# Kernel optimization log

Hardware: AMD Instinct MI355X
Metric: run time of the kernel (lower is better)

The kernel has to match this reference:

```python
import jax, jax.numpy as jnp
import numpy as np

N = 50000      # nodes
E = 1600000    # message edges (avg degree 32)
EQ = 500000    # link-prediction query edges
IN, HID, OUT, FCH = 128, 128, 64, 256
ALPHA = 0.5


def setup_inputs() -> dict:
    key = jax.random.key(0)
    ks = jax.random.split(key, 8)
    def p(k, shape):
        fan_in = shape[0]
        return jax.random.normal(k, shape, jnp.float32) * (1.0 / np.sqrt(fan_in))
    return {
        "x": jax.random.normal(ks[0], (N, IN), jnp.float32),
        "edge_index": jax.random.randint(ks[1], (2, E), 0, N),
        "edge_label_index": jax.random.randint(ks[2], (2, EQ), 0, N),
        "W1": p(ks[3], (IN, HID)),  "b1": jnp.zeros((HID,), jnp.float32),
        "W2": p(ks[4], (HID, OUT)), "b2": jnp.zeros((OUT,), jnp.float32),
        "Wf1": p(ks[5], (IN, FCH)), "bf1": jnp.zeros((FCH,), jnp.float32),
        "Wf2": p(ks[6], (FCH, OUT)), "bf2": jnp.zeros((OUT,), jnp.float32),
    }


def reference(x, edge_index, edge_label_index, W1, b1, W2, b2, Wf1, bf1, Wf2, bf2):
    n = x.shape[0]
    # GCN self-loops + symmetric normalization (PyG GCNConv defaults)
    loop = jnp.arange(n)
    src = jnp.concatenate([edge_index[0], loop])
    dst = jnp.concatenate([edge_index[1], loop])
    deg = jax.ops.segment_sum(jnp.ones_like(dst, jnp.float32), dst, num_segments=n)
    dinv = jnp.where(deg > 0, jax.lax.rsqrt(deg), 0.0)
    norm = dinv[src] * dinv[dst]  # [E+N]

    def gcn(h, W, b):
        h = h @ W                                  # transform first (PyG order)
        msg = norm[:, None] * h[src]               # gather + scale per edge
        return jax.ops.segment_sum(msg, dst, num_segments=n) + b

    x_gcn = jax.nn.relu(gcn(x, W1, b1))
    x_gcn = gcn(x_gcn, W2, b2)
    x_fc = jax.nn.relu(x @ Wf1 + bf1) @ Wf2 + bf2
    z = x_gcn * (1.0 - ALPHA) + x_fc * ALPHA       # [N, OUT]
    # edge dot-product decode
    return jnp.sum(z[edge_label_index[0]] * z[edge_label_index[1]], axis=1)
```

## Files before the change

kernel.cpp:

```cpp
#include <hip/hip_runtime.h>

#define FIN   128
#define FHID  128
#define FOUT  64
#define FFC   256
#define CHUNK 4096
#define BKBITS 7
#define BKN   128
#define ECAP  4608

typedef __attribute__((ext_vector_type(8))) short          bf16x8;
typedef __attribute__((ext_vector_type(4))) float          f32x4;
typedef __attribute__((ext_vector_type(2))) float          f32x2;
typedef __attribute__((ext_vector_type(8))) unsigned short u16x8;

static __device__ __forceinline__ unsigned short f2bf(float f) {
    unsigned int u = __float_as_uint(f);
    u = (u + 0x7fffu + ((u >> 16) & 1u)) >> 16;
    return (unsigned short)u;
}
static __device__ __forceinline__ float bf2f(unsigned short s) {
    return __uint_as_float(((unsigned int)s) << 16);
}
static __device__ __forceinline__ void accum_fp8(float* acc, uint4 g) {
    f32x2 p;
    p = __builtin_amdgcn_cvt_pk_f32_fp8(g.x, false); acc[0]  += p.x; acc[1]  += p.y;
    p = __builtin_amdgcn_cvt_pk_f32_fp8(g.x, true);  acc[2]  += p.x; acc[3]  += p.y;
    p = __builtin_amdgcn_cvt_pk_f32_fp8(g.y, false); acc[4]  += p.x; acc[5]  += p.y;
    p = __builtin_amdgcn_cvt_pk_f32_fp8(g.y, true);  acc[6]  += p.x; acc[7]  += p.y;
    p = __builtin_amdgcn_cvt_pk_f32_fp8(g.z, false); acc[8]  += p.x; acc[9]  += p.y;
    p = __builtin_amdgcn_cvt_pk_f32_fp8(g.z, true);  acc[10] += p.x; acc[11] += p.y;
    p = __builtin_amdgcn_cvt_pk_f32_fp8(g.w, false); acc[12] += p.x; acc[13] += p.y;
    p = __builtin_amdgcn_cvt_pk_f32_fp8(g.w, true);  acc[14] += p.x; acc[15] += p.y;
}

__global__ __launch_bounds__(256) void binA_cvt_kernel(
    const int* __restrict__ src, const int* __restrict__ dst,
    int* __restrict__ bcur, unsigned int* __restrict__ ebuf, int E, int NBA,
    const float* __restrict__ W1, const float* __restrict__ W2,
    const float* __restrict__ Wf1, const float* __restrict__ Wf2,
    unsigned short* __restrict__ w1t, unsigned short* __restrict__ w2t,
    unsigned short* __restrict__ wf1t, unsigned short* __restrict__ wf2t)
{
    int t = threadIdx.x;
    if (blockIdx.x >= NBA) {
        long i = (long)(blockIdx.x - NBA) * 256 + t;
        if (i < 16384) {
            int k = (int)i >> 7, n = (int)i & 127;
            w1t[n * 128 + k] = f2bf(W1[i]);
        } else if (i < 24576) {
            int j = (int)i - 16384; int k = j >> 6, n = j & 63;
            w2t[n * 128 + k] = f2bf(W2[j]);
        } else if (i < 57344) {
            int j = (int)i - 24576; int k = j >> 8, n = j & 255;
            wf1t[n * 128 + k] = f2bf(Wf1[j]);
        } else if (i < 73728) {
            int j = (int)i - 57344; int k = j >> 6, n = j & 63;
            wf2t[n * 256 + k] = f2bf(Wf2[j]);
        }
        return;
    }
    __shared__ int hist[512];
    __shared__ int rstart[512];
    __shared__ int lcur[512];
    hist[t] = 0; hist[t + 256] = 0; lcur[t] = 0; lcur[t + 256] = 0;
    __syncthreads();
    int e0 = blockIdx.x * CHUNK;
    int e1 = min(e0 + CHUNK, E);
    for (int e = e0 + t; e < e1; e += 256)
        atomicAdd(&hist[dst[e] >> BKBITS], 1);
    __syncthreads();
    if (hist[t])       rstart[t]       = atomicAdd(&bcur[t],       hist[t]);
    if (hist[t + 256]) rstart[t + 256] = atomicAdd(&bcur[t + 256], hist[t + 256]);
    __syncthreads();
    for (int e = e0 + t; e < e1; e += 256) {
        int s = src[e], d = dst[e];
        int b = d >> BKBITS;
        int pos = rstart[b] + atomicAdd(&lcur[b], 1);
        if (pos < ECAP)
            ebuf[(size_t)b * ECAP + pos] =
                ((unsigned)s << BKBITS) | ((unsigned)d & (BKN - 1));
    }
}

__global__ __launch_bounds__(256) void binB_fc_kernel(
    const unsigned int* __restrict__ ebuf, const int* __restrict__ bcnt,
    int2* __restrict__ rp2, int* __restrict__ col, float* __restrict__ dinv,
    unsigned char* __restrict__ xs, int N, int NBK,
    const float* __restrict__ X,
    const unsigned short* __restrict__ B1T,
    const unsigned short* __restrict__ B2T,
    const float* __restrict__ bias1, const float* __restrict__ bias2,
    unsigned short* __restrict__ C, int M)
{
    __shared__ __align__(16) unsigned char smem[49152];
    const int tid = threadIdx.x;

    if (blockIdx.x < NBK) {
        int* cnt           = (int*)smem;
        int* tmp           = (int*)(smem + 512);
        int* ccur          = (int*)(smem + 1536);
        int* scur          = (int*)(smem + 2048);
        float* sdinv       = (float*)(smem + 3072);
        unsigned int* skey = (unsigned int*)(smem + 3584);
        int* colLds        = (int*)(smem + 22016);
        int b = blockIdx.x;
        int t = tid;
        size_t base = (size_t)b * ECAP;
        int ne = min(bcnt[b], ECAP);
        if (t < 128) cnt[t] = 0;
        scur[t] = 0;
        __syncthreads();
        for (int e = t; e < ne; e += 256) {
            unsigned int k = ebuf[base + e];
            atomicAdd(&cnt[k & (BKN - 1)], 1);
            atomicAdd(&scur[k >> 15], 1);
        }
        __syncthreads();
        int c = (t < 128) ? cnt[t] : 0;
        tmp[t] = c;
        __syncthreads();
        int acc = c;
        for (int off = 1; off < 128; off <<= 1) {
            int a = (t >= off) ? tmp[t - off] : 0;
            __syncthreads();
            acc += a; tmp[t] = acc;
            __syncthreads();
        }
        if (t < 128) {
            float di = rsqrtf((float)c + 1.0f);
            sdinv[t] = di;
            int node = b * BKN + t;
            int st = (int)base + acc - c;
            if (node < N) { dinv[node] = di; rp2[node] = make_int2(st, st + c); }
            ccur[t] = acc - c;
        }
        __syncthreads();
        int sv = scur[t];
        tmp[t] = sv;
        __syncthreads();
        int sacc = sv;
        for (int off = 1; off < 256; off <<= 1) {
            int a = (t >= off) ? tmp[t - off] : 0;
            __syncthreads();
            sacc += a; tmp[t] = sacc;
            __syncthreads();
        }
        scur[t] = sacc - sv;
        __syncthreads();
        for (int e = t; e < ne; e += 256) {
            unsigned int k = ebuf[base + e];
            int pos = atomicAdd(&scur[k >> 15], 1);
            skey[pos] = k;
        }
        __syncthreads();
        for (int w = 0; w < ne; w += 256) {
            int e = w + t;
            if (e < ne) {
                unsigned int k = skey[e];
                int pos = atomicAdd(&ccur[k & (BKN - 1)], 1);
                colLds[pos] = (int)(k >> BKBITS);
            }
            __syncthreads();
        }
        for (int e = t; e < ne; e += 256)
            col[base + e] = colLds[e];
        int nl0 = t >> 3;
        int f0 = (t & 7) << 4;
        #pragma unroll
        for (int it = 0; it < 4; it++) {
            int nl = it * 32 + nl0;
            int gn = b * BKN + nl;
            if (gn >= N) continue;
            float d2 = sdinv[nl];
            const float* xr = X + (size_t)gn * FIN + f0;
            float4 va = *(const float4*)(xr);
            float4 vb = *(const float4*)(xr + 4);
            float4 vc = *(const float4*)(xr + 8);
            float4 vd = *(const float4*)(xr + 12);
            float f[16] = { va.x * d2, va.y * d2, va.z * d2, va.w * d2,
                            vb.x * d2, vb.y * d2, vb.z * d2, vb.w * d2,
                            vc.x * d2, vc.y * d2, vc.z * d2, vc.w * d2,
                            vd.x * d2, vd.y * d2, vd.z * d2, vd.w * d2 };
            uint4 w;
            w.x = 0; w.y = 0; w.z = 0; w.w = 0;
            w.x = __builtin_amdgcn_cvt_pk_fp8_f32(f[0],  f[1],  w.x, false);
            w.x = __builtin_amdgcn_cvt_pk_fp8_f32(f[2],  f[3],  w.x, true);
            w.y = __builtin_amdgcn_cvt_pk_fp8_f32(f[4],  f[5],  w.y, false);
            w.y = __builtin_amdgcn_cvt_pk_fp8_f32(f[6],  f[7],  w.y, true);
            w.z = __builtin_amdgcn_cvt_pk_fp8_f32(f[8],  f[9],  w.z, false);
            w.z = __builtin_amdgcn_cvt_pk_fp8_f32(f[10], f[11], w.z, true);
            w.w = __builtin_amdgcn_cvt_pk_fp8_f32(f[12], f[13], w.w, false);
            w.w = __builtin_amdgcn_cvt_pk_fp8_f32(f[14], f[15], w.w, true);
            *(uint4*)(xs + (size_t)gn * 128 + f0) = w;
        }
        return;
    }

    unsigned short* lds = (unsigned short*)smem;
    const int lane = tid & 63;
    const int wave = tid >> 6;
    const int m = lane & 15;
    const int q = lane >> 4;
    const int rowbase = (blockIdx.x - NBK) * 64 + wave * 16;
    const int row = rowbase + m;

    float4 av[8] = {};
    {
        const float* arow = X + (size_t)row * FIN + q * 8;
        if (row < M) {
            #pragma unroll
            for (int kk = 0; kk < 4; kk++) {
                av[2 * kk]     = *(const float4*)(arow + kk * 32);
                av[2 * kk + 1] = *(const float4*)(arow + kk * 32 + 4);
            }
        }
    }

    #pragma unroll 2
    for (int i = tid; i < 2048; i += 256) {
        int n = i >> 4, sl = i & 15;
        ((u16x8*)lds)[(n << 4) | (sl ^ (n & 7))] = ((const u16x8*)B1T)[i];
    }
    __syncthreads();

    f32x4 acc[16] = {};
    for (int k0 = 0; k0 < 128; k0 += 32) {
        int kk = k0 >> 5;
        float4 a0 = av[2 * kk], a1 = av[2 * kk + 1];
        bf16x8 a;
        a[0] = (short)f2bf(a0.x); a[1] = (short)f2bf(a0.y);
        a[2] = (short)f2bf(a0.z); a[3] = (short)f2bf(a0.w);
        a[4] = (short)f2bf(a1.x); a[5] = (short)f2bf(a1.y);
        a[6] = (short)f2bf(a1.z); a[7] = (short)f2bf(a1.w);
        int sl = q + (k0 >> 3);
        #pragma unroll
        for (int c = 0; c < 8; c++) {
            int cc = c * 16 + m;
            bf16x8 b = ((const bf16x8*)lds)[(cc << 4) | (sl ^ (cc & 7))];
            acc[c] = __builtin_amdgcn_mfma_f32_16x16x32_bf16(a, b, acc[c], 0, 0, 0);
        }
    }
    __syncthreads();
    #pragma unroll 2
    for (int i = tid; i < 2048; i += 256) {
        int n = i >> 4, sl = i & 15;
        ((u16x8*)lds)[(n << 4) | (sl ^ (n & 7))] = ((const u16x8*)B1T)[2048 + i];
    }
    __syncthreads();
    for (int k0 = 0; k0 < 128; k0 += 32) {
        int kk = k0 >> 5;
        float4 a0 = av[2 * kk], a1 = av[2 * kk + 1];
        bf16x8 a;
        a[0] = (short)f2bf(a0.x); a[1] = (short)f2bf(a0.y);
        a[2] = (short)f2bf(a0.z); a[3] = (short)f2bf(a0.w);
        a[4] = (short)f2bf(a1.x); a[5] = (short)f2bf(a1.y);
        a[6] = (short)f2bf(a1.z); a[7] = (short)f2bf(a1.w);
        int sl = q + (k0 >> 3);
        #pragma unroll
        for (int c = 0; c < 8; c++) {
            int cc = c * 16 + m;
            bf16x8 b = ((const bf16x8*)lds)[(cc << 4) | (sl ^ (cc & 7))];
            acc[8 + c] = __builtin_amdgcn_mfma_f32_16x16x32_bf16(a, b, acc[8 + c], 0, 0, 0);
        }
    }
    __syncthreads();
    #pragma unroll
    for (int c = 0; c < 16; c++) {
        int cc = c * 16 + m;
        float bv = bias1[cc];
        #pragma unroll
        for (int r = 0; r < 4; r++) {
            int rr = wave * 16 + q * 4 + r;
            float v = fmaxf(acc[c][r] + bv, 0.f);
            lds[rr * 256 + ((((cc >> 3) ^ (rr & 7)) << 3) | (cc & 7))] = f2bf(v);
        }
    }
    for (int i = tid; i < 1024; i += 256) {
        int n = i >> 4, sl = i & 15;
        ((u16x8*)lds)[2048 + ((n << 4) | (sl ^ (n & 7)))] =
            ((const u16x8*)B2T)[n * 32 + sl];
    }
    __syncthreads();

    f32x4 acc2[4] = {};
    {
        int rr = wave * 16 + m;
        for (int k0 = 0; k0 < 128; k0 += 32) {
            int sl = q + (k0 >> 3);
            bf16x8 a = ((const bf16x8*)lds)[(rr << 5) | (sl ^ (rr & 7))];
            #pragma unroll
            for (int c = 0; c < 4; c++) {
                int cc = c * 16 + m;
                bf16x8 b = ((const bf16x8*)lds)[2048 + ((cc << 4) | (sl ^ (cc & 7)))];
                acc2[c] = __builtin_amdgcn_mfma_f32_16x16x32_bf16(a, b, acc2[c], 0, 0, 0);
            }
        }
    }
    __syncthreads();
    for (int i = tid; i < 1024; i += 256) {
        int n = i >> 4, sl = i & 15;
        ((u16x8*)lds)[2048 + ((n << 4) | (sl ^ (n & 7)))] =
            ((const u16x8*)B2T)[n * 32 + 16 + sl];
    }
    __syncthreads();
    {
        int rr = wave * 16 + m;
        for (int k0 = 128; k0 < 256; k0 += 32) {
            int sla = q + (k0 >> 3);
            int slb = q + ((k0 - 128) >> 3);
            bf16x8 a = ((const bf16x8*)lds)[(rr << 5) | (sla ^ (rr & 7))];
            #pragma unroll
            for (int c = 0; c < 4; c++) {
                int cc = c * 16 + m;
                bf16x8 b = ((const bf16x8*)lds)[2048 + ((cc << 4) | (slb ^ (cc & 7)))];
                acc2[c] = __builtin_amdgcn_mfma_f32_16x16x32_bf16(a, b, acc2[c], 0, 0, 0);
            }
        }
    }
    __syncthreads();

    constexpr int ROWB = 4 * 16 * 2 + 16;
    unsigned char* wbase = (unsigned char*)lds + wave * 16 * ROWB;
    #pragma unroll
    for (int c = 0; c < 4; c++) {
        int lc = c * 16 + m;
        float bv = bias2[lc];
        #pragma unroll
        for (int r = 0; r < 4; r++)
            ((unsigned short*)(wbase + (q * 4 + r) * ROWB))[lc] =
                f2bf(acc2[c][r] + bv);
    }
    #pragma unroll
    for (int p = 0; p < 2; p++) {
        int r2 = p * 8 + (lane >> 3);
        int bo = (lane & 7) * 16;
        int gr = rowbase + r2;
        if (gr < M) {
            uint4 v = *(const uint4*)(wbase + r2 * ROWB + bo);
            *(uint4*)((unsigned char*)C + (size_t)gr * FOUT * 2 + bo) = v;
        }
    }
}

__global__ __launch_bounds__(256) void pull1_kernel(
    const unsigned char* __restrict__ xs, const int2* __restrict__ rp2,
    const int* __restrict__ col, const float* __restrict__ dinv,
    unsigned short* __restrict__ aggx, int N)
{
    int tid = threadIdx.x;
    int node = blockIdx.x * 32 + (tid >> 3);
    if (node >= N) return;
    int f0 = (tid & 7) << 4;
    const unsigned char* base = xs + f0;
    float di = dinv[node];
    int2 se = rp2[node];
    float acc[16] = {};
    accum_fp8(acc, *(const uint4*)(base + (size_t)node * 128));
    int e = se.x, end = se.y;
    for (; e + 4 <= end; e += 4) {
        int s0 = col[e], s1 = col[e + 1], s2 = col[e + 2], s3 = col[e + 3];
        uint4 g0 = *(const uint4*)(base + (size_t)s0 * 128);
        uint4 g1 = *(const uint4*)(base + (size_t)s1 * 128);
        uint4 g2 = *(const uint4*)(base + (size_t)s2 * 128);
        uint4 g3 = *(const uint4*)(base + (size_t)s3 * 128);
        accum_fp8(acc, g0); accum_fp8(acc, g1);
        accum_fp8(acc, g2); accum_fp8(acc, g3);
    }
    for (; e < end; e++)
        accum_fp8(acc, *(const uint4*)(base + (size_t)col[e] * 128));
    u16x8 o0, o1;
    #pragma unroll
    for (int j = 0; j < 8; j++) {
        o0[j] = f2bf(di * acc[j]);
        o1[j] = f2bf(di * acc[8 + j]);
    }
    *(u16x8*)(aggx + (size_t)node * FIN + f0)     = o0;
    *(u16x8*)(aggx + (size_t)node * FIN + f0 + 8) = o1;
}

__global__ __launch_bounds__(256) void gcn_kernel(
    const unsigned short* __restrict__ A,
    const unsigned short* __restrict__ B1T,
    const unsigned short* __restrict__ B2T,
    const float* __restrict__ bias1,
    const float* __restrict__ rowscale,
    unsigned short* __restrict__ C, int M)
{
    __shared__ __align__(16) unsigned short lds[16384];
    const int tid  = threadIdx.x;
    const int lane = tid & 63;
    const int wave = tid >> 6;
    const int m = lane & 15;
    const int q = lane >> 4;
    const int rowbase = blockIdx.x * 64 + wave * 16;
    const int row = rowbase + m;

    bf16x8 areg[4] = {};
    {
        const unsigned short* arow = A + (size_t)row * FIN + q * 8;
        if (row < M) {
            #pragma unroll
            for (int kk = 0; kk < 4; kk++)
                areg[kk] = *(const bf16x8*)(arow + kk * 32);
        }
    }

    #pragma unroll 2
    for (int i = tid; i < 2048; i += 256) {
        int n = i >> 4, sl = i & 15;
        ((u16x8*)lds)[(n << 4) | (sl ^ (n & 7))] = ((const u16x8*)B1T)[i];
    }
    __syncthreads();

    f32x4 acc[8] = {};
    for (int k0 = 0; k0 < 128; k0 += 32) {
        bf16x8 a = areg[k0 >> 5];
        int sl = q + (k0 >> 3);
        #pragma unroll
        for (int c = 0; c < 8; c++) {
            int cc = c * 16 + m;
            bf16x8 b = ((const bf16x8*)lds)[(cc << 4) | (sl ^ (cc & 7))];
            acc[c] = __builtin_amdgcn_mfma_f32_16x16x32_bf16(a, b, acc[c], 0, 0, 0);
        }
    }
    __syncthreads();

    #pragma unroll
    for (int c = 0; c < 8; c++) {
        int cc = c * 16 + m;
        float bv = bias1[cc];
        #pragma unroll
        for (int r = 0; r < 4; r++) {
            int rr = wave * 16 + q * 4 + r;
            float v = fmaxf(acc[c][r] + bv, 0.f);
            lds[rr * 128 + ((((cc >> 3) ^ (rr & 7)) << 3) | (cc & 7))] = f2bf(v);
        }
    }
    for (int i = tid; i < 1024; i += 256) {
        int n = i >> 4, sl = i & 15;
        ((u16x8*)lds)[1024 + ((n << 4) | (sl ^ (n & 7)))] = ((const u16x8*)B2T)[i];
    }
    __syncthreads();

    f32x4 acc2[4] = {};
    {
        int rr = wave * 16 + m;
        for (int k0 = 0; k0 < 128; k0 += 32) {
            int sl = q + (k0 >> 3);
            bf16x8 a = ((const bf16x8*)lds)[(rr << 4) | (sl ^ (rr & 7))];
            #pragma unroll
            for (int c = 0; c < 4; c++) {
                int cc = c * 16 + m;
                bf16x8 b = ((const bf16x8*)lds)[1024 + ((cc << 4) | (sl ^ (cc & 7)))];
                acc2[c] = __builtin_amdgcn_mfma_f32_16x16x32_bf16(a, b, acc2[c], 0, 0, 0);
            }
        }
    }
    float rs[4];
    #pragma unroll
    for (int r = 0; r < 4; r++) {
        int gr = rowbase + q * 4 + r;
        rs[r] = (gr < M) ? rowscale[gr] : 1.0f;
    }
    __syncthreads();

    constexpr int ROWB = 4 * 16 * 2 + 16;
    unsigned char* wbase = (unsigned char*)lds + wave * 16 * ROWB;
    #pragma unroll
    for (int c = 0; c < 4; c++) {
        int lc = c * 16 + m;
        #pragma unroll
        for (int r = 0; r < 4; r++)
            ((unsigned short*)(wbase + (q * 4 + r) * ROWB))[lc] =
                f2bf(acc2[c][r] * rs[r]);
    }
    #pragma unroll
    for (int p = 0; p < 2; p++) {
        int r2 = p * 8 + (lane >> 3);
        int bo = (lane & 7) * 16;
        int gr = rowbase + r2;
        if (gr < M) {
            uint4 v = *(const uint4*)(wbase + r2 * ROWB + bo);
            *(uint4*)((unsigned char*)C + (size_t)gr * FOUT * 2 + bo) = v;
        }
    }
}

__global__ __launch_bounds__(256) void pull2_kernel(
    const unsigned short* __restrict__ t2s, const int2* __restrict__ rp2,
    const int* __restrict__ col, const float* __restrict__ dinv,
    const unsigned short* __restrict__ xfc, const float* __restrict__ b2,
    unsigned short* __restrict__ zbf, int N)
{
    int tid = threadIdx.x;
    int node = blockIdx.x * 32 + (tid >> 3);
    if (node >= N) return;
    int f0 = (tid & 7) << 3;
    const unsigned short* base = t2s + f0;
    float di = dinv[node];
    u16x8 xv = *(const u16x8*)(xfc + (size_t)node * FOUT + f0);
    float4 bb0 = *(const float4*)(b2 + f0);
    float4 bb1 = *(const float4*)(b2 + f0 + 4);
    u16x8 own = *(const u16x8*)(base + (size_t)node * FOUT);
    float acc[8];
    #pragma unroll
    for (int j = 0; j < 8; j++) acc[j] = bf2f(own[j]);
    int2 se = rp2[node];
    int e = se.x, end = se.y;
    for (; e + 4 <= end; e += 4) {
        int s0 = col[e], s1 = col[e + 1], s2 = col[e + 2], s3 = col[e + 3];
        u16x8 v0 = *(const u16x8*)(base + (size_t)s0 * FOUT);
        u16x8 v1 = *(const u16x8*)(base + (size_t)s1 * FOUT);
        u16x8 v2 = *(const u16x8*)(base + (size_t)s2 * FOUT);
        u16x8 v3 = *(const u16x8*)(base + (size_t)s3 * FOUT);
        #pragma unroll
        for (int j = 0; j < 8; j++)
            acc[j] += (bf2f(v0[j]) + bf2f(v1[j])) + (bf2f(v2[j]) + bf2f(v3[j]));
    }
    for (; e < end; e++) {
        u16x8 v = *(const u16x8*)(base + (size_t)col[e] * FOUT);
        #pragma unroll
        for (int j = 0; j < 8; j++) acc[j] += bf2f(v[j]);
    }
    float bv[8] = { bb0.x, bb0.y, bb0.z, bb0.w, bb1.x, bb1.y, bb1.z, bb1.w };
    u16x8 o;
    #pragma unroll
    for (int j = 0; j < 8; j++)
        o[j] = f2bf(0.5f * (di * acc[j] + bv[j]) + 0.5f * bf2f(xv[j]));
    *(u16x8*)(zbf + (size_t)node * FOUT + f0) = o;
}

__global__ void decode_kernel(
    const unsigned short* __restrict__ zbf, const int* __restrict__ eli,
    float* __restrict__ out, int Q)
{
    int tid = blockIdx.x * blockDim.x + threadIdx.x;
    int q = tid >> 3;
    if (q >= Q) return;
    int lane = tid & 7;
    int a = eli[q];
    int b = eli[Q + q];
    u16x8 va = *(const u16x8*)(zbf + (size_t)a * FOUT + lane * 8);
    u16x8 vb = *(const u16x8*)(zbf + (size_t)b * FOUT + lane * 8);
    float s = 0.f;
    #pragma unroll
    for (int j = 0; j < 8; j++) s += bf2f(va[j]) * bf2f(vb[j]);
    s += __shfl_down(s, 4, 8);
    s += __shfl_down(s, 2, 8);
    s += __shfl_down(s, 1, 8);
    if (lane == 0) out[q] = s;
}

extern "C" void kernel_launch(void* const* d_in, const int* in_sizes, int n_in,
                              void* d_out, int out_size, void* d_ws, size_t ws_size,
                              hipStream_t stream)
{
    const float* x   = (const float*)d_in[0];
    const int*   ei  = (const int*)  d_in[1];
    const int*   eli = (const int*)  d_in[2];
    const float* W1  = (const float*)d_in[3];
    const float* b1  = (const float*)d_in[4];
    const float* W2  = (const float*)d_in[5];
    const float* b2  = (const float*)d_in[6];
    const float* Wf1 = (const float*)d_in[7];
    const float* bf1 = (const float*)d_in[8];
    const float* Wf2 = (const float*)d_in[9];
    const float* bf2 = (const float*)d_in[10];
    float* out = (float*)d_out;

    const int N = in_sizes[0] / FIN;
    const int E = in_sizes[1] / 2;
    const int Q = in_sizes[2] / 2;
    const int* src = ei;
    const int* dst = ei + E;
    const int NBK = (N + BKN - 1) >> BKBITS;
    const int NBA = (E + CHUNK - 1) / CHUNK;
    const int NCV = 73728 / 256;
    const int NFC = (N + 63) / 64;

    char* p = (char*)d_ws;
    float* dinv = (float*)p;             p += (size_t)N * 4;
    int2*  rp2  = (int2*)p;              p += (size_t)N * 8;
    int*   bcur = (int*)p;               p += 2048;
    unsigned short* w1t  = (unsigned short*)p; p += FIN * FHID * 2;
    unsigned short* w2t  = (unsigned short*)p; p += FHID * FOUT * 2;
    unsigned short* wf1t = (unsigned short*)p; p += FIN * FFC * 2;
    unsigned short* wf2t = (unsigned short*)p; p += FFC * FOUT * 2;
    unsigned short* xfc = (unsigned short*)p;  p += (size_t)N * FOUT * 2;
    unsigned char* xs = (unsigned char*)p;     p += (size_t)N * 128;
    unsigned int* ebuf = (unsigned int*)p;  p += (size_t)NBK * ECAP * 4;
    int*   col  = (int*)p;               p += (size_t)NBK * ECAP * 4;
    unsigned short* aggx = (unsigned short*)p; p += (size_t)N * FIN * 2;
    unsigned short* t2s  = (unsigned short*)p; p += (size_t)N * FOUT * 2;
    unsigned short* zbf  = (unsigned short*)p; p += (size_t)N * FOUT * 2;

    const int TB = 256;

    hipMemsetAsync(bcur, 0, 2048, stream);

    binA_cvt_kernel<<<NBA + NCV, TB, 0, stream>>>(
        src, dst, bcur, ebuf, E, NBA,
        W1, W2, Wf1, Wf2, w1t, w2t, wf1t, wf2t);

    binB_fc_kernel<<<NBK + NFC, TB, 0, stream>>>(
        ebuf, bcur, rp2, col, dinv, xs, N, NBK,
        x, wf1t, wf2t, bf1, bf2, xfc, N);

    pull1_kernel<<<(N + 31) / 32, TB, 0, stream>>>(xs, rp2, col, dinv, aggx, N);

    gcn_kernel<<<(N + 63) / 64, TB, 0, stream>>>(
        aggx, w1t, w2t, b1, dinv, t2s, N);

    pull2_kernel<<<(N + 31) / 32, TB, 0, stream>>>(
        t2s, rp2, col, dinv, xfc, b2, zbf, N);

    {
        long total = (long)Q * 8;
        decode_kernel<<<(int)((total + TB - 1) / TB), TB, 0, stream>>>(
            zbf, eli, out, Q);
    }
}
```

Baseline: 242.4 us.

## Co-schedule edge binning with FC MLP and split weight conversion into own kernel

Weight conversion moves into its own small kernel. Edge pass A (histogram binning) now shares a launch with the FC MLP blocks, and bin pass B (CSR build plus fp8 x scaling) runs as a separate kernel afterwards. The binning pass also loads its 16 src/dst pairs per thread into registers once instead of reading global memory twice. The aim is to overlap the memory-bound binning with the compute-bound FC GEMM and cut redundant index loads, at the cost of one extra kernel launch.

```diff
diff --git a/kernel.cpp b/kernel.cpp
--- a/kernel.cpp
+++ b/kernel.cpp
@@ -34,59 +34,31 @@
     p = __builtin_amdgcn_cvt_pk_f32_fp8(g.w, true);  acc[14] += p.x; acc[15] += p.y;
 }
 
-__global__ __launch_bounds__(256) void binA_cvt_kernel(
-    const int* __restrict__ src, const int* __restrict__ dst,
-    int* __restrict__ bcur, unsigned int* __restrict__ ebuf, int E, int NBA,
+__global__ __launch_bounds__(256) void cvt_kernel(
     const float* __restrict__ W1, const float* __restrict__ W2,
     const float* __restrict__ Wf1, const float* __restrict__ Wf2,
     unsigned short* __restrict__ w1t, unsigned short* __restrict__ w2t,
     unsigned short* __restrict__ wf1t, unsigned short* __restrict__ wf2t)
 {
-    int t = threadIdx.x;
-    if (blockIdx.x >= NBA) {
-        long i = (long)(blockIdx.x - NBA) * 256 + t;
-        if (i < 16384) {
-            int k = (int)i >> 7, n = (int)i & 127;
-            w1t[n * 128 + k] = f2bf(W1[i]);
-        } else if (i < 24576) {
-            int j = (int)i - 16384; int k = j >> 6, n = j & 63;
-            w2t[n * 128 + k] = f2bf(W2[j]);
-        } else if (i < 57344) {
-            int j = (int)i - 24576; int k = j >> 8, n = j & 255;
-            wf1t[n * 128 + k] = f2bf(Wf1[j]);
-        } else if (i < 73728) {
-            int j = (int)i - 57344; int k = j >> 6, n = j & 63;
-            wf2t[n * 256 + k] = f2bf(Wf2[j]);
-        }
-        return;
-    }
-    __shared__ int hist[512];
-    __shared__ int rstart[512];
-    __shared__ int lcur[512];
-    hist[t] = 0; hist[t + 256] = 0; lcur[t] = 0; lcur[t + 256] = 0;
-    __syncthreads();
-    int e0 = blockIdx.x * CHUNK;
-    int e1 = min(e0 + CHUNK, E);
-    for (int e = e0 + t; e < e1; e += 256)
-        atomicAdd(&hist[dst[e] >> BKBITS], 1);
-    __syncthreads();
-    if (hist[t])       rstart[t]       = atomicAdd(&bcur[t],       hist[t]);
-    if (hist[t + 256]) rstart[t + 256] = atomicAdd(&bcur[t + 256], hist[t + 256]);
-    __syncthreads();
-    for (int e = e0 + t; e < e1; e += 256) {
-        int s = src[e], d = dst[e];
-        int b = d >> BKBITS;
-        int pos = rstart[b] + atomicAdd(&lcur[b], 1);
-        if (pos < ECAP)
-            ebuf[(size_t)b * ECAP + pos] =
-                ((unsigned)s << BKBITS) | ((unsigned)d & (BKN - 1));
-    }
-}
-
-__global__ __launch_bounds__(256) void binB_fc_kernel(
-    const unsigned int* __restrict__ ebuf, const int* __restrict__ bcnt,
-    int2* __restrict__ rp2, int* __restrict__ col, float* __restrict__ dinv,
-    unsigned char* __restrict__ xs, int N, int NBK,
+    long i = (long)blockIdx.x * 256 + threadIdx.x;
+    if (i < 16384) {
+        int k = (int)i >> 7, n = (int)i & 127;
+        w1t[n * 128 + k] = f2bf(W1[i]);
+    } else if (i < 24576) {
+        int j = (int)i - 16384; int k = j >> 6, n = j & 63;
+        w2t[n * 128 + k] = f2bf(W2[j]);
+    } else if (i < 57344) {
+        int j = (int)i - 24576; int k = j >> 8, n = j & 255;
+        wf1t[n * 128 + k] = f2bf(Wf1[j]);
+    } else if (i < 73728) {
+        int j = (int)i - 57344; int k = j >> 6, n = j & 63;
+        wf2t[n * 256 + k] = f2bf(Wf2[j]);
+    }
+}
+
+__global__ __launch_bounds__(256) void binA_fc_kernel(
+    const int* __restrict__ src, const int* __restrict__ dst,
+    int* __restrict__ bcur, unsigned int* __restrict__ ebuf, int E, int NBA,
     const float* __restrict__ X,
     const unsigned short* __restrict__ B1T,
     const unsigned short* __restrict__ B2T,
@@ -96,103 +68,41 @@
     __shared__ __align__(16) unsigned char smem[49152];
     const int tid = threadIdx.x;
 
-    if (blockIdx.x < NBK) {
-        int* cnt           = (int*)smem;
-        int* tmp           = (int*)(smem + 512);
-        int* ccur          = (int*)(smem + 1536);
-        int* scur          = (int*)(smem + 2048);
-        float* sdinv       = (float*)(smem + 3072);
-        unsigned int* skey = (unsigned int*)(smem + 3584);
-        int* colLds        = (int*)(smem + 22016);
-        int b = blockIdx.x;
+    if (blockIdx.x < NBA) {
+        int* hist   = (int*)smem;
+        int* rstart = (int*)(smem + 2048);
+        int* lcur   = (int*)(smem + 4096);
         int t = tid;
-        size_t base = (size_t)b * ECAP;
-        int ne = min(bcnt[b], ECAP);
-        if (t < 128) cnt[t] = 0;
-        scur[t] = 0;
-        __syncthreads();
-        for (int e = t; e < ne; e += 256) {
-            unsigned int k = ebuf[base + e];
-            atomicAdd(&cnt[k & (BKN - 1)], 1);
-            atomicAdd(&scur[k >> 15], 1);
-        }
-        __syncthreads();
-        int c = (t < 128) ? cnt[t] : 0;
-        tmp[t] = c;
-        __syncthreads();
-        int acc = c;
-        for (int off = 1; off < 128; off <<= 1) {
-            int a = (t >= off) ? tmp[t - off] : 0;
-            __syncthreads();
-            acc += a; tmp[t] = acc;
-            __syncthreads();
-        }
-        if (t < 128) {
-            float di = rsqrtf((float)c + 1.0f);
-            sdinv[t] = di;
-            int node = b * BKN + t;
-            int st = (int)base + acc - c;
-            if (node < N) { dinv[node] = di; rp2[node] = make_int2(st, st + c); }
-            ccur[t] = acc - c;
-        }
-        __syncthreads();
-        int sv = scur[t];
-        tmp[t] = sv;
-        __syncthreads();
-        int sacc = sv;
-        for (int off = 1; off < 256; off <<= 1) {
-            int a = (t >= off) ? tmp[t - off] : 0;
-            __syncthreads();
-            sacc += a; tmp[t] = sacc;
-            __syncthreads();
-        }
-        scur[t] = sacc - sv;
-        __syncthreads();
-        for (int e = t; e < ne; e += 256) {
-            unsigned int k = ebuf[base + e];
-            int pos = atomicAdd(&scur[k >> 15], 1);
-            skey[pos] = k;
-        }
-        __syncthreads();
-        for (int w = 0; w < ne; w += 256) {
-            int e = w + t;
-            if (e < ne) {
-                unsigned int k = skey[e];
-                int pos = atomicAdd(&ccur[k & (BKN - 1)], 1);
-                colLds[pos] = (int)(k >> BKBITS);
+        hist[t] = 0; hist[t + 256] = 0; lcur[t] = 0; lcur[t + 256] = 0;
+        __syncthreads();
+        int e0 = blockIdx.x * CHUNK;
+        int cnt_e = min(CHUNK, E - e0);
+        int sreg[16], dreg[16];
+        #pragma unroll
+        for (int i = 0; i < 16; i++) {
+            int o = t + i * 256;
+            bool ok = o < cnt_e;
+            sreg[i] = ok ? src[e0 + o] : 0;
+            dreg[i] = ok ? dst[e0 + o] : 0;
+            if (ok) ;
+        }
+        #pragma unroll
+        for (int i = 0; i < 16; i++)
+            if (t + i * 256 < cnt_e) atomicAdd(&hist[dreg[i] >> BKBITS], 1);
+        __syncthreads();
+        if (hist[t])       rstart[t]       = atomicAdd(&bcur[t],       hist[t]);
+        if (hist[t + 256]) rstart[t + 256] = atomicAdd(&bcur[t + 256], hist[t + 256]);
+        __syncthreads();
+        #pragma unroll
+        for (int i = 0; i < 16; i++) {
+            if (t + i * 256 < cnt_e) {
+                int s = sreg[i], d = dreg[i];
+                int b = d >> BKBITS;
+                int pos = rstart[b] + atomicAdd(&lcur[b], 1);
+                if (pos < ECAP)
+                    ebuf[(size_t)b * ECAP + pos] =
+                        ((unsigned)s << BKBITS) | ((unsigned)d & (BKN - 1));
             }
-            __syncthreads();
-        }
-        for (int e = t; e < ne; e += 256)
-            col[base + e] = colLds[e];
-        int nl0 = t >> 3;
-        int f0 = (t & 7) << 4;
-        #pragma unroll
-        for (int it = 0; it < 4; it++) {
-            int nl = it * 32 + nl0;
-            int gn = b * BKN + nl;
-            if (gn >= N) continue;
-            float d2 = sdinv[nl];
-            const float* xr = X + (size_t)gn * FIN + f0;
-            float4 va = *(const float4*)(xr);
-            float4 vb = *(const float4*)(xr + 4);
-            float4 vc = *(const float4*)(xr + 8);
-            float4 vd = *(const float4*)(xr + 12);
-            float f[16] = { va.x * d2, va.y * d2, va.z * d2, va.w * d2,
-                            vb.x * d2, vb.y * d2, vb.z * d2, vb.w * d2,
-                            vc.x * d2, vc.y * d2, vc.z * d2, vc.w * d2,
-                            vd.x * d2, vd.y * d2, vd.z * d2, vd.w * d2 };
-            uint4 w;
-            w.x = 0; w.y = 0; w.z = 0; w.w = 0;
-            w.x = __builtin_amdgcn_cvt_pk_fp8_f32(f[0],  f[1],  w.x, false);
-            w.x = __builtin_amdgcn_cvt_pk_fp8_f32(f[2],  f[3],  w.x, true);
-            w.y = __builtin_amdgcn_cvt_pk_fp8_f32(f[4],  f[5],  w.y, false);
-            w.y = __builtin_amdgcn_cvt_pk_fp8_f32(f[6],  f[7],  w.y, true);
-            w.z = __builtin_amdgcn_cvt_pk_fp8_f32(f[8],  f[9],  w.z, false);
-            w.z = __builtin_amdgcn_cvt_pk_fp8_f32(f[10], f[11], w.z, true);
-            w.w = __builtin_amdgcn_cvt_pk_fp8_f32(f[12], f[13], w.w, false);
-            w.w = __builtin_amdgcn_cvt_pk_fp8_f32(f[14], f[15], w.w, true);
-            *(uint4*)(xs + (size_t)gn * 128 + f0) = w;
         }
         return;
     }
@@ -202,7 +112,7 @@
     const int wave = tid >> 6;
     const int m = lane & 15;
     const int q = lane >> 4;
-    const int rowbase = (blockIdx.x - NBK) * 64 + wave * 16;
+    const int rowbase = (blockIdx.x - NBA) * 64 + wave * 16;
     const int row = rowbase + m;
 
     float4 av[8] = {};
@@ -340,6 +250,111 @@
             uint4 v = *(const uint4*)(wbase + r2 * ROWB + bo);
             *(uint4*)((unsigned char*)C + (size_t)gr * FOUT * 2 + bo) = v;
         }
+    }
+}
+
+__global__ __launch_bounds__(256) void binB_kernel(
+    const unsigned int* __restrict__ ebuf, const int* __restrict__ bcnt,
+    int2* __restrict__ rp2, int* __restrict__ col, float* __restrict__ dinv,
+    const float* __restrict__ x, unsigned char* __restrict__ xs, int N)
+{
+    __shared__ __align__(16) unsigned char smem[40448];
+    int* cnt           = (int*)smem;
+    int* tmp           = (int*)(smem + 512);
+    int* ccur          = (int*)(smem + 1536);
+    int* scur          = (int*)(smem + 2048);
+    float* sdinv       = (float*)(smem + 3072);
+    unsigned int* skey = (unsigned int*)(smem + 3584);
+    int* colLds        = (int*)(smem + 22016);
+    int b = blockIdx.x;
+    int t = threadIdx.x;
+    size_t base = (size_t)b * ECAP;
+    int ne = min(bcnt[b], ECAP);
+    if (t < 128) cnt[t] = 0;
+    scur[t] = 0;
+    __syncthreads();
+    for (int e = t; e < ne; e += 256) {
+        unsigned int k = ebuf[base + e];
+        atomicAdd(&cnt[k & (BKN - 1)], 1);
+        atomicAdd(&scur[k >> 15], 1);
+    }
+    __syncthreads();
+    int c = (t < 128) ? cnt[t] : 0;
+    tmp[t] = c;
+    __syncthreads();
+    int acc = c;
+    for (int off = 1; off < 128; off <<= 1) {
+        int a = (t >= off) ? tmp[t - off] : 0;
+        __syncthreads();
+        acc += a; tmp[t] = acc;
+        __syncthreads();
+    }
+    if (t < 128) {
+        float di = rsqrtf((float)c + 1.0f);
+        sdinv[t] = di;
+        int node = b * BKN + t;
+        int st = (int)base + acc - c;
+        if (node < N) { dinv[node] = di; rp2[node] = make_int2(st, st + c); }
+        ccur[t] = acc - c;
+    }
+    __syncthreads();
+    int sv = scur[t];
+    tmp[t] = sv;
+    __syncthreads();
+    int sacc = sv;
+    for (int off = 1; off < 256; off <<= 1) {
+        int a = (t >= off) ? tmp[t - off] : 0;
+        __syncthreads();
+        sacc += a; tmp[t] = sacc;
+        __syncthreads();
+    }
+    scur[t] = sacc - sv;
+    __syncthreads();
+    for (int e = t; e < ne; e += 256) {
+        unsigned int k = ebuf[base + e];
+        int pos = atomicAdd(&scur[k >> 15], 1);
+        skey[pos] = k;
+    }
+    __syncthreads();
+    for (int w = 0; w < ne; w += 256) {
+        int e = w + t;
+        if (e < ne) {
+            unsigned int k = skey[e];
+            int pos = atomicAdd(&ccur[k & (BKN - 1)], 1);
+            colLds[pos] = (int)(k >> BKBITS);
+        }
+        __syncthreads();
+    }
+    for (int e = t; e < ne; e += 256)
+        col[base + e] = colLds[e];
+    int nl0 = t >> 3;
+    int f0 = (t & 7) << 4;
+    #pragma unroll
+    for (int it = 0; it < 4; it++) {
+        int nl = it * 32 + nl0;
+        int gn = b * BKN + nl;
+        if (gn >= N) continue;
+        float d2 = sdinv[nl];
+        const float* xr = x + (size_t)gn * FIN + f0;
+        float4 va = *(const float4*)(xr);
+        float4 vb = *(const float4*)(xr + 4);
+        float4 vc = *(const float4*)(xr + 8);
+        float4 vd = *(const float4*)(xr + 12);
+        float f[16] = { va.x * d2, va.y * d2, va.z * d2, va.w * d2,
+                        vb.x * d2, vb.y * d2, vb.z * d2, vb.w * d2,
+                        vc.x * d2, vc.y * d2, vc.z * d2, vc.w * d2,
+                        vd.x * d2, vd.y * d2, vd.z * d2, vd.w * d2 };
+        uint4 w;
+        w.x = 0; w.y = 0; w.z = 0; w.w = 0;
+        w.x = __builtin_amdgcn_cvt_pk_fp8_f32(f[0],  f[1],  w.x, false);
+        w.x = __builtin_amdgcn_cvt_pk_fp8_f32(f[2],  f[3],  w.x, true);
+        w.y = __builtin_amdgcn_cvt_pk_fp8_f32(f[4],  f[5],  w.y, false);
+        w.y = __builtin_amdgcn_cvt_pk_fp8_f32(f[6],  f[7],  w.y, true);
+        w.z = __builtin_amdgcn_cvt_pk_fp8_f32(f[8],  f[9],  w.z, false);
+        w.z = __builtin_amdgcn_cvt_pk_fp8_f32(f[10], f[11], w.z, true);
+        w.w = __builtin_amdgcn_cvt_pk_fp8_f32(f[12], f[13], w.w, false);
+        w.w = __builtin_amdgcn_cvt_pk_fp8_f32(f[14], f[15], w.w, true);
+        *(uint4*)(xs + (size_t)gn * 128 + f0) = w;
     }
 }
 
@@ -599,13 +614,14 @@
 
     hipMemsetAsync(bcur, 0, 2048, stream);
 
-    binA_cvt_kernel<<<NBA + NCV, TB, 0, stream>>>(
+    cvt_kernel<<<NCV, TB, 0, stream>>>(
+        W1, W2, Wf1, Wf2, w1t, w2t, wf1t, wf2t);
+
+    binA_fc_kernel<<<NBA + NFC, TB, 0, stream>>>(
         src, dst, bcur, ebuf, E, NBA,
-        W1, W2, Wf1, Wf2, w1t, w2t, wf1t, wf2t);
-
-    binB_fc_kernel<<<NBK + NFC, TB, 0, stream>>>(
-        ebuf, bcur, rp2, col, dinv, xs, N, NBK,
         x, wf1t, wf2t, bf1, bf2, xfc, N);
+
+    binB_kernel<<<NBK, TB, 0, stream>>>(ebuf, bcur, rp2, col, dinv, x, xs, N);
 
     pull1_kernel<<<(N + 31) / 32, TB, 0, stream>>>(xs, rp2, col, dinv, aggx, N);
 
```

After: 236.8 us. 1.02x faster.
